# Kernel optimization log

Measured on AMD Instinct MI355X. Metric: run time of the kernel, lower is better.

## Reference

```python
import jax, jax.numpy as jnp
import numpy as np

# LIF dynamics constants (match init_kwargs)
STEPS = 20          # T // dt
DT = 1.0
TAU_M = 20.0
TAU_S = 5.0
THRESH = 1.0
SUR_ALPHA = 10.0    # surrogate-gradient sharpness (stand-in for custom spikeprop bwd)

@jax.custom_vjp
def spike_fn(v):
    # Heaviside threshold; nondifferentiable, custom vjp supplies surrogate grad
    return (v >= THRESH).astype(v.dtype)

def _spike_fwd(v):
    return spike_fn(v), v

def _spike_bwd(v, g):
    # fast-sigmoid (SuperSpike) surrogate derivative centered at threshold
    sur = 1.0 / (1.0 + SUR_ALPHA * jnp.abs(v - THRESH)) ** 2
    return (g * sur,)

spike_fn.defvjp(_spike_fwd, _spike_bwd)


def setup_inputs() -> dict:
    key = jax.random.key(0)
    k1, k2 = jax.random.split(key)
    # Bernoulli(0.1) rate-coded input spike train: [steps, batch, input_dim]
    x = (jax.random.uniform(k1, (STEPS, 512, 2048)) < 0.1).astype(jnp.float32)
    # nn.init.normal_(weight, mean=mu, std=mu) with mu=0.1; W: [output_dim, input_dim]
    W = 0.1 + 0.1 * jax.random.normal(k2, (2048, 2048), dtype=jnp.float32)
    return {"x": x, "W": W}


def reference(x, W):
    # x: [steps, batch, input_dim] spikes; W: [out, in]
    a_m = 1.0 - DT / TAU_M   # membrane decay
    a_s = 1.0 - DT / TAU_S   # synaptic decay
    B = x.shape[1]
    O = W.shape[0]

    def step(carry, x_t):
        V, I = carry                       # [B, O] each
        V_new = a_m * V + (DT / TAU_M) * I # leaky integration of synaptic current
        s = spike_fn(V_new)                # threshold crossing -> spikes
        V_new = V_new * (1.0 - s)          # reset-to-zero on spike
        I_new = a_s * I + x_t @ W.T        # synaptic current driven by input spikes
        return (V_new, I_new), s

    init = (jnp.zeros((B, O), x.dtype), jnp.zeros((B, O), x.dtype))
    _, spikes = jax.lax.scan(step, init, x)
    return spikes  # [steps, batch, output_dim]
```

## Files before the change

kernel.cpp:

```cpp
#include <hip/hip_runtime.h>
#include <stdint.h>


#define STEPS  20
#define BATCH  512
#define DIM    2048

#define XQ_OFF   0ULL
#define WQ_OFF   20971520ULL
#define C_OFF    37748736ULL

#define GLOBAL_AS __attribute__((address_space(1)))
#define LDS_AS    __attribute__((address_space(3)))

typedef int v4i  __attribute__((ext_vector_type(4)));
typedef int v16i __attribute__((ext_vector_type(16)));


__global__ __launch_bounds__(256)
void prep_x_kernel(const float* __restrict__ x, char* __restrict__ wsb)
{
    const int bid = blockIdx.x;
    const int kc = bid & 31, mt = bid >> 5;
    const int tid = threadIdx.x;
    char* outb = wsb + (size_t)bid * 8192;
#pragma unroll
    for (int it = 0; it < 8; ++it) {
        const int idx = it * 256 + tid;
        const int mm = idx >> 4;
        const int kk4 = (idx & 15) << 2;
        const float4 v = *reinterpret_cast<const float4*>(
            x + (size_t)(mt * 128 + mm) * DIM + kc * 64 + kk4);
        uchar4 o;
        o.x = (v.x != 0.0f); o.y = (v.y != 0.0f);
        o.z = (v.z != 0.0f); o.w = (v.w != 0.0f);
        *reinterpret_cast<uchar4*>(
            outb + (((kk4 >> 4) * 128 + mm) << 4) + (kk4 & 15)) = o;
    }
}

__global__ __launch_bounds__(256)
void prep_w_kernel(const float* __restrict__ W, char* __restrict__ wsb)
{
    const int bid = blockIdx.x;
    const int kc = bid & 31, nt = bid >> 5;
    const int tid = threadIdx.x;
    char* wqb = wsb + WQ_OFF;
#pragma unroll
    for (int it = 0; it < 8; ++it) {
        const int idx = it * 256 + tid;
        const int nn = idx >> 4;
        const int kk4 = (idx & 15) << 2;
        const float4 v = *reinterpret_cast<const float4*>(
            W + (size_t)(nt * 128 + nn) * DIM + kc * 64 + kk4);
        int dg[4][4];
        const float* vp = &v.x;
#pragma unroll
        for (int c = 0; c < 4; ++c) {
            long long q = __double2ll_rn((double)vp[c] * 2147483648.0);
#pragma unroll
            for (int j = 0; j < 3; ++j) {
                int d = (int)(q & 255);
                if (d >= 128) d -= 256;
                dg[c][j] = d;
                q = (q - d) >> 8;
            }
            dg[c][3] = (int)q;
        }
        const size_t sub = (size_t)(((kk4 >> 4) * 128 + nn) << 4) + (kk4 & 15);
#pragma unroll
        for (int j = 0; j < 4; ++j) {
            uchar4 o;
            o.x = (unsigned char)(dg[0][j] & 255);
            o.y = (unsigned char)(dg[1][j] & 255);
            o.z = (unsigned char)(dg[2][j] & 255);
            o.w = (unsigned char)(dg[3][j] & 255);
            *reinterpret_cast<uchar4*>(
                wqb + ((size_t)((j * 16 + nt) * 32 + kc)) * 8192 + sub) = o;
        }
    }
}

__global__ __launch_bounds__(256, 4)
void gemm_i8_kernel(const char* __restrict__ wsb_c, short* __restrict__ cp,
                    int nt0, int ntc_cnt, int no)
{
    __shared__ __align__(16) char lds[2][16384];

    const int bid = blockIdx.x;
    const int mt = bid % 80;
    const int rest = bid / 80;
    const int ntc = rest % ntc_cnt;
    const int limb = rest / ntc_cnt;

    const int tid = threadIdx.x;
    const int lane = tid & 63, w = tid >> 6;
    const int kh = lane >> 5, ln = lane & 31;
    const int wy = w & 1, wx = w >> 1;

    const char* abase = wsb_c + XQ_OFF + ((size_t)mt * 32) * 8192;
    const char* bbase = wsb_c + WQ_OFF
        + ((size_t)((limb * 16 + nt0 + ntc) * 32)) * 8192;

    const int aoff = ((kh * 128) + wy * 64 + ln) << 4;
    const int boff = ((kh * 128) + wx * 64 + ln) << 4;
    const int stg = (w * 2) * 1024 + (lane << 4);

    v16i acc00, acc01, acc10, acc11;
#pragma unroll
    for (int r = 0; r < 16; ++r) {
        acc00[r] = 0; acc01[r] = 0; acc10[r] = 0; acc11[r] = 0;
    }

    LDS_AS char* l0 = (LDS_AS char*)(&lds[0][0]);
    LDS_AS char* l1 = (LDS_AS char*)(&lds[1][0]);

#pragma unroll
    for (int i = 0; i < 2; ++i) {
        __builtin_amdgcn_global_load_lds(
            (const GLOBAL_AS void*)(abase + stg + i * 1024),
            (LDS_AS void*)(l0 + (w * 2 + i) * 1024), 16, 0, 0);
        __builtin_amdgcn_global_load_lds(
            (const GLOBAL_AS void*)(bbase + stg + i * 1024),
            (LDS_AS void*)(l0 + 8192 + (w * 2 + i) * 1024), 16, 0, 0);
    }

    for (int kc = 0; kc < 32; ++kc) {
        __syncthreads();
        const int cur = kc & 1;
        if (kc + 1 < 32) {
            LDS_AS char* ldst = (kc & 1) ? l0 : l1;
            const size_t src = (size_t)(kc + 1) * 8192 + stg;
#pragma unroll
            for (int i = 0; i < 2; ++i) {
                __builtin_amdgcn_global_load_lds(
                    (const GLOBAL_AS void*)(abase + src + i * 1024),
                    (LDS_AS void*)(ldst + (w * 2 + i) * 1024), 16, 0, 0);
                __builtin_amdgcn_global_load_lds(
                    (const GLOBAL_AS void*)(bbase + src + i * 1024),
                    (LDS_AS void*)(ldst + 8192 + (w * 2 + i) * 1024), 16, 0, 0);
            }
        }
        const char* A = &lds[cur][0];
        const char* B = &lds[cur][8192];
#pragma unroll
        for (int s = 0; s < 2; ++s) {
            const v4i a0 = *reinterpret_cast<const v4i*>(A + aoff + s * 4096);
            const v4i a1 = *reinterpret_cast<const v4i*>(A + aoff + 512 + s * 4096);
            const v4i b0 = *reinterpret_cast<const v4i*>(B + boff + s * 4096);
            const v4i b1 = *reinterpret_cast<const v4i*>(B + boff + 512 + s * 4096);
            acc00 = __builtin_amdgcn_mfma_i32_32x32x32_i8(a0, b0, acc00, 0, 0, 0);
            acc01 = __builtin_amdgcn_mfma_i32_32x32x32_i8(a0, b1, acc01, 0, 0, 0);
            acc10 = __builtin_amdgcn_mfma_i32_32x32x32_i8(a1, b0, acc10, 0, 0, 0);
            acc11 = __builtin_amdgcn_mfma_i32_32x32x32_i8(a1, b1, acc11, 0, 0, 0);
        }
    }

    short* cpl = cp + (size_t)limb * 10240 * no;
    const int m_base = mt * 128 + wy * 64;
    const int o_base = ntc * 128 + wx * 64 + ln;
#pragma unroll
    for (int r = 0; r < 16; ++r) {
        const int row = (r & 3) + ((r >> 2) << 3) + (kh << 2);
        const size_t m0 = (size_t)(m_base + row) * no;
        const size_t m1 = (size_t)(m_base + 32 + row) * no;
        cpl[m0 + o_base]      = (short)acc00[r];
        cpl[m0 + o_base + 32] = (short)acc01[r];
        cpl[m1 + o_base]      = (short)acc10[r];
        cpl[m1 + o_base + 32] = (short)acc11[r];
    }
}

__global__ __launch_bounds__(256)
void lif_kernel(const short* __restrict__ cp, float* __restrict__ out,
                int o0, int no, int shift)
{
    const int g = blockIdx.x * 256 + threadIdx.x;
    const int b = g >> shift;
    const int oq = g & ((1 << shift) - 1);
    const int o_local = oq << 2;
    const size_t plane = (size_t)10240 * no;

    const double A_M = 1.0 - 1.0 / 20.0;
    const double DTM = 1.0 / 20.0;
    const double A_S = 1.0 - 1.0 / 5.0;
    double V[4], I[4];
#pragma unroll
    for (int u = 0; u < 4; ++u) { V[u] = 0.0; I[u] = 0.0; }

#pragma unroll
    for (int t = 0; t < STEPS; ++t) {
        const size_t ix = (size_t)(t * BATCH + b) * no + o_local;
        const short4 c0 = *reinterpret_cast<const short4*>(cp + ix);
        const short4 c1 = *reinterpret_cast<const short4*>(cp + plane + ix);
        const short4 c2 = *reinterpret_cast<const short4*>(cp + 2 * plane + ix);
        const short4 c3 = *reinterpret_cast<const short4*>(cp + 3 * plane + ix);
        const short* p0 = &c0.x; const short* p1 = &c1.x;
        const short* p2 = &c2.x; const short* p3 = &c3.x;
        float4 s;
        float* sp = &s.x;
#pragma unroll
        for (int u = 0; u < 4; ++u) {
            const long long tot = (long long)p0[u]
                + ((long long)p1[u] << 8)
                + ((long long)p2[u] << 16)
                + ((long long)p3[u] << 24);
            const double val = (double)tot * 4.6566128730773926e-10;
            V[u] = A_M * V[u] + DTM * I[u];
            float sv = 0.0f;
            if (V[u] >= 1.0) { sv = 1.0f; V[u] = 0.0; }
            sp[u] = sv;
            I[u] = A_S * I[u] + val;
        }
        *reinterpret_cast<float4*>(
            out + (size_t)(t * BATCH + b) * DIM + o0 + o_local) = s;
    }
}


#define B_TILE 2
#define O_TILE 256
#define NT     512
#define KT     32
#define NSLAB  (DIM / KT)
#define ROWB   1024

__global__ __launch_bounds__(256)
void transpose_kernel(const float* __restrict__ W, float* __restrict__ WT)
{
    __shared__ float tile[64][65];
    const int tid = threadIdx.x;
    const int c4 = (tid & 15) * 4;
    const int rr = tid >> 4;
    const int k0 = blockIdx.x * 64, o0 = blockIdx.y * 64;
#pragma unroll
    for (int i = 0; i < 64; i += 16) {
        const float4 v = *reinterpret_cast<const float4*>(
            W + (size_t)(o0 + rr + i) * DIM + k0 + c4);
        tile[c4 + 0][rr + i] = v.x;
        tile[c4 + 1][rr + i] = v.y;
        tile[c4 + 2][rr + i] = v.z;
        tile[c4 + 3][rr + i] = v.w;
    }
    __syncthreads();
#pragma unroll
    for (int i = 0; i < 64; i += 16) {
        float4 v;
        v.x = tile[rr + i][c4 + 0];
        v.y = tile[rr + i][c4 + 1];
        v.z = tile[rr + i][c4 + 2];
        v.w = tile[rr + i][c4 + 3];
        *reinterpret_cast<float4*>(
            WT + (size_t)(k0 + rr + i) * DIM + o0 + c4) = v;
    }
}

__global__ __launch_bounds__(NT, 6)
void snn_lif_kernel(const float* __restrict__ x,
                    const float* __restrict__ WT,
                    float* __restrict__ out)
{
    __shared__ __align__(16) float wlds[(KT * ROWB) / 4];

    const int tid  = threadIdx.x;
    const int lane = tid & 63;
    const int w    = tid >> 6;
    const int bl   = w & 1;
    const int tq   = w >> 1;
    const int o_blk = blockIdx.x & 7;
    const int b_blk = blockIdx.x >> 3;
    const int b  = b_blk * B_TILE + bl;
    const int o0 = o_blk * O_TILE;

    double acc[5][4];
#pragma unroll
    for (int tt = 0; tt < 5; ++tt)
#pragma unroll
        for (int u = 0; u < 4; ++u) acc[tt][u] = 0.0;

    const int kl = lane & 31;
    float xr[5];
#pragma unroll
    for (int m = 0; m < 5; ++m)
        xr[m] = x[((size_t)(tq * 5 + m) * BATCH + b) * DIM + kl];

    const char*   gb   = (const char*)wlds + (lane << 4);
    LDS_AS char*  ldsb = (LDS_AS char*)wlds;
    const float*  wsrc = WT + o0 + (lane << 2);

    for (int kt = 0; kt < NSLAB; ++kt) {
        const int k0 = kt * KT;
        __syncthreads();
#pragma unroll
        for (int it = 0; it < 4; ++it) {
            const int r = w + it * 8;
            __builtin_amdgcn_global_load_lds(
                (const GLOBAL_AS void*)(wsrc + (size_t)(k0 + r) * DIM),
                (LDS_AS void*)(ldsb + r * ROWB), 16, 0, 0);
        }
        unsigned mk[5];
#pragma unroll
        for (int m = 0; m < 5; ++m)
            mk[m] = (unsigned)__ballot(xr[m] != 0.0f);
        __syncthreads();
        if (kt + 1 < NSLAB) {
            const int k1 = k0 + KT;
#pragma unroll
            for (int m = 0; m < 5; ++m)
                xr[m] = x[((size_t)(tq * 5 + m) * BATCH + b) * DIM + k1 + kl];
        }
#pragma unroll
        for (int m = 0; m < 5; ++m) {
            unsigned msk = mk[m];
            while (msk & (msk - 1)) {
                const int r0 = __builtin_ctz(msk); msk &= msk - 1;
                const int r1 = __builtin_ctz(msk); msk &= msk - 1;
                const float4 va = *reinterpret_cast<const float4*>(gb + (r0 << 10));
                const float4 vb = *reinterpret_cast<const float4*>(gb + (r1 << 10));
                acc[m][0] += (double)va.x; acc[m][1] += (double)va.y;
                acc[m][2] += (double)va.z; acc[m][3] += (double)va.w;
                acc[m][0] += (double)vb.x; acc[m][1] += (double)vb.y;
                acc[m][2] += (double)vb.z; acc[m][3] += (double)vb.w;
            }
            if (msk) {
                const int r = __builtin_ctz(msk);
                const float4 wv = *reinterpret_cast<const float4*>(gb + (r << 10));
                acc[m][0] += (double)wv.x; acc[m][1] += (double)wv.y;
                acc[m][2] += (double)wv.z; acc[m][3] += (double)wv.w;
            }
        }
    }

    const double A_M = 1.0 - 1.0 / 20.0;
    const double DTM = 1.0 / 20.0;
    const double A_S = 1.0 - 1.0 / 5.0;

    __syncthreads();
    double2* hand = reinterpret_cast<double2*>(wlds);
    const int hbase = bl * 256 + (lane << 2);
    const size_t obase = (size_t)o0 + (lane << 2);

    for (int seg = 0; seg < 4; ++seg) {
        if (tq == seg) {
            double V[4], I[4];
            if (seg == 0) {
#pragma unroll
                for (int u = 0; u < 4; ++u) { V[u] = 0.0; I[u] = 0.0; }
            } else {
#pragma unroll
                for (int u = 0; u < 4; ++u) {
                    const double2 h = hand[hbase + u];
                    V[u] = h.x; I[u] = h.y;
                }
            }
#pragma unroll
            for (int tt = 0; tt < 5; ++tt) {
                const int t = seg * 5 + tt;
                float4 s;
                float* sp = &s.x;
#pragma unroll
                for (int u = 0; u < 4; ++u) {
                    V[u] = A_M * V[u] + DTM * I[u];
                    float sv = 0.0f;
                    if (V[u] >= 1.0) { sv = 1.0f; V[u] = 0.0; }
                    sp[u] = sv;
                    I[u] = A_S * I[u] + acc[tt][u];
                }
                *reinterpret_cast<float4*>(
                    out + ((size_t)t * BATCH + b) * DIM + obase) = s;
            }
            if (seg < 3) {
#pragma unroll
                for (int u = 0; u < 4; ++u)
                    hand[hbase + u] = make_double2(V[u], I[u]);
            }
        }
        __syncthreads();
    }
}


extern "C" void kernel_launch(void* const* d_in, const int* in_sizes, int n_in,
                              void* d_out, int out_size, void* d_ws, size_t ws_size,
                              hipStream_t stream) {
    const float* x = (const float*)d_in[0];
    const float* W = (const float*)d_in[1];
    float* out = (float*)d_out;
    char* wsb = (char*)d_ws;

    int no = 0, shift = 0;
    if      (ws_size >= C_OFF + 81920ULL * 2048) { no = 2048; shift = 9; }
    else if (ws_size >= C_OFF + 81920ULL * 1024) { no = 1024; shift = 8; }
    else if (ws_size >= C_OFF + 81920ULL * 512)  { no = 512;  shift = 7; }
    else if (ws_size >= C_OFF + 81920ULL * 256)  { no = 256;  shift = 6; }
    else if (ws_size >= C_OFF + 81920ULL * 128)  { no = 128;  shift = 5; }

    if (no) {
        prep_x_kernel<<<2560, 256, 0, stream>>>(x, wsb);
        prep_w_kernel<<<512, 256, 0, stream>>>(W, wsb);
        short* cp = (short*)(wsb + C_OFF);
        const int ntc_cnt = no / 128;
        for (int nt0 = 0; nt0 < 16; nt0 += ntc_cnt) {
            gemm_i8_kernel<<<4 * ntc_cnt * 80, 256, 0, stream>>>(
                (const char*)wsb, cp, nt0, ntc_cnt, no);
            lif_kernel<<<no / 2, 256, 0, stream>>>(
                (const short*)cp, out, nt0 * 128, no, shift);
        }
    } else {
        float* WT = (float*)d_ws;
        dim3 tb(256);
        dim3 tg(DIM / 64, DIM / 64);
        transpose_kernel<<<tg, tb, 0, stream>>>(W, WT);
        const int grid = (BATCH / B_TILE) * (DIM / O_TILE);
        snn_lif_kernel<<<grid, NT, 0, stream>>>(x, WT, out);
    }
}
```

Baseline: 338.0 us.

## Enlarge int8 GEMM block tile to 256x128 and stage W-limb writes through LDS

```diff
diff --git a/kernel.cpp b/kernel.cpp
--- a/kernel.cpp
+++ b/kernel.cpp
@@ -42,6 +42,7 @@
 __global__ __launch_bounds__(256)
 void prep_w_kernel(const float* __restrict__ W, char* __restrict__ wsb)
 {
+    __shared__ __align__(16) char pl[4][8192];
     const int bid = blockIdx.x;
     const int kc = bid & 31, nt = bid >> 5;
     const int tid = threadIdx.x;
@@ -67,7 +68,7 @@
             }
             dg[c][3] = (int)q;
         }
-        const size_t sub = (size_t)(((kk4 >> 4) * 128 + nn) << 4) + (kk4 & 15);
+        const int sub = (((kk4 >> 4) * 128 + nn) << 4) + (kk4 & 15);
 #pragma unroll
         for (int j = 0; j < 4; ++j) {
             uchar4 o;
@@ -75,36 +76,48 @@
             o.y = (unsigned char)(dg[1][j] & 255);
             o.z = (unsigned char)(dg[2][j] & 255);
             o.w = (unsigned char)(dg[3][j] & 255);
-            *reinterpret_cast<uchar4*>(
-                wqb + ((size_t)((j * 16 + nt) * 32 + kc)) * 8192 + sub) = o;
-        }
-    }
-}
-
-__global__ __launch_bounds__(256, 4)
+            *reinterpret_cast<uchar4*>(&pl[j][sub]) = o;
+        }
+    }
+    __syncthreads();
+#pragma unroll
+    for (int j = 0; j < 4; ++j) {
+        char* dst = wqb + ((size_t)((j * 16 + nt) * 32 + kc)) * 8192;
+#pragma unroll
+        for (int rep = 0; rep < 2; ++rep) {
+            const int off = (rep * 256 + tid) * 16;
+            *reinterpret_cast<int4*>(dst + off) =
+                *reinterpret_cast<const int4*>(&pl[j][off]);
+        }
+    }
+}
+
+__global__ __launch_bounds__(512, 4)
 void gemm_i8_kernel(const char* __restrict__ wsb_c, short* __restrict__ cp,
                     int nt0, int ntc_cnt, int no)
 {
-    __shared__ __align__(16) char lds[2][16384];
+    __shared__ __align__(16) char lds[2][24576];
 
     const int bid = blockIdx.x;
-    const int mt = bid % 80;
-    const int rest = bid / 80;
+    const int mtb = bid % 40;
+    const int rest = bid / 40;
     const int ntc = rest % ntc_cnt;
     const int limb = rest / ntc_cnt;
 
     const int tid = threadIdx.x;
     const int lane = tid & 63, w = tid >> 6;
     const int kh = lane >> 5, ln = lane & 31;
-    const int wy = w & 1, wx = w >> 1;
-
-    const char* abase = wsb_c + XQ_OFF + ((size_t)mt * 32) * 8192;
+    const int wy = w & 3, wx = w >> 2;
+
+    const char* abase0 = wsb_c + XQ_OFF + ((size_t)(2 * mtb) * 32) * 8192;
+    const char* abase1 = abase0 + (size_t)32 * 8192;
     const char* bbase = wsb_c + WQ_OFF
         + ((size_t)((limb * 16 + nt0 + ntc) * 32)) * 8192;
 
-    const int aoff = ((kh * 128) + wy * 64 + ln) << 4;
-    const int boff = ((kh * 128) + wx * 64 + ln) << 4;
-    const int stg = (w * 2) * 1024 + (lane << 4);
+    const int atile = (wy >> 1) * 8192;
+    const int aoffl = ((kh * 128) + (wy & 1) * 64 + ln) << 4;
+    const int boff  = ((kh * 128) + wx * 64 + ln) << 4;
+    const int stg = w * 1024 + (lane << 4);
 
     v16i acc00, acc01, acc10, acc11;
 #pragma unroll
@@ -115,15 +128,15 @@
     LDS_AS char* l0 = (LDS_AS char*)(&lds[0][0]);
     LDS_AS char* l1 = (LDS_AS char*)(&lds[1][0]);
 
-#pragma unroll
-    for (int i = 0; i < 2; ++i) {
-        __builtin_amdgcn_global_load_lds(
-            (const GLOBAL_AS void*)(abase + stg + i * 1024),
-            (LDS_AS void*)(l0 + (w * 2 + i) * 1024), 16, 0, 0);
-        __builtin_amdgcn_global_load_lds(
-            (const GLOBAL_AS void*)(bbase + stg + i * 1024),
-            (LDS_AS void*)(l0 + 8192 + (w * 2 + i) * 1024), 16, 0, 0);
-    }
+    __builtin_amdgcn_global_load_lds(
+        (const GLOBAL_AS void*)(abase0 + stg),
+        (LDS_AS void*)(l0 + w * 1024), 16, 0, 0);
+    __builtin_amdgcn_global_load_lds(
+        (const GLOBAL_AS void*)(abase1 + stg),
+        (LDS_AS void*)(l0 + 8192 + w * 1024), 16, 0, 0);
+    __builtin_amdgcn_global_load_lds(
+        (const GLOBAL_AS void*)(bbase + stg),
+        (LDS_AS void*)(l0 + 16384 + w * 1024), 16, 0, 0);
 
     for (int kc = 0; kc < 32; ++kc) {
         __syncthreads();
@@ -131,22 +144,22 @@
         if (kc + 1 < 32) {
             LDS_AS char* ldst = (kc & 1) ? l0 : l1;
             const size_t src = (size_t)(kc + 1) * 8192 + stg;
-#pragma unroll
-            for (int i = 0; i < 2; ++i) {
-                __builtin_amdgcn_global_load_lds(
-                    (const GLOBAL_AS void*)(abase + src + i * 1024),
-                    (LDS_AS void*)(ldst + (w * 2 + i) * 1024), 16, 0, 0);
-                __builtin_amdgcn_global_load_lds(
-                    (const GLOBAL_AS void*)(bbase + src + i * 1024),
-                    (LDS_AS void*)(ldst + 8192 + (w * 2 + i) * 1024), 16, 0, 0);
-            }
-        }
-        const char* A = &lds[cur][0];
-        const char* B = &lds[cur][8192];
+            __builtin_amdgcn_global_load_lds(
+                (const GLOBAL_AS void*)(abase0 + src),
+                (LDS_AS void*)(ldst + w * 1024), 16, 0, 0);
+            __builtin_amdgcn_global_load_lds(
+                (const GLOBAL_AS void*)(abase1 + src),
+                (LDS_AS void*)(ldst + 8192 + w * 1024), 16, 0, 0);
+            __builtin_amdgcn_global_load_lds(
+                (const GLOBAL_AS void*)(bbase + src),
+                (LDS_AS void*)(ldst + 16384 + w * 1024), 16, 0, 0);
+        }
+        const char* A = &lds[cur][atile];
+        const char* B = &lds[cur][16384];
 #pragma unroll
         for (int s = 0; s < 2; ++s) {
-            const v4i a0 = *reinterpret_cast<const v4i*>(A + aoff + s * 4096);
-            const v4i a1 = *reinterpret_cast<const v4i*>(A + aoff + 512 + s * 4096);
+            const v4i a0 = *reinterpret_cast<const v4i*>(A + aoffl + s * 4096);
+            const v4i a1 = *reinterpret_cast<const v4i*>(A + aoffl + 512 + s * 4096);
             const v4i b0 = *reinterpret_cast<const v4i*>(B + boff + s * 4096);
             const v4i b1 = *reinterpret_cast<const v4i*>(B + boff + 512 + s * 4096);
             acc00 = __builtin_amdgcn_mfma_i32_32x32x32_i8(a0, b0, acc00, 0, 0, 0);
@@ -157,7 +170,7 @@
     }
 
     short* cpl = cp + (size_t)limb * 10240 * no;
-    const int m_base = mt * 128 + wy * 64;
+    const int m_base = mtb * 256 + wy * 64;
     const int o_base = ntc * 128 + wx * 64 + ln;
 #pragma unroll
     for (int r = 0; r < 16; ++r) {
@@ -401,7 +414,7 @@
         short* cp = (short*)(wsb + C_OFF);
         const int ntc_cnt = no / 128;
         for (int nt0 = 0; nt0 < 16; nt0 += ntc_cnt) {
-            gemm_i8_kernel<<<4 * ntc_cnt * 80, 256, 0, stream>>>(
+            gemm_i8_kernel<<<40 * ntc_cnt * 4, 512, 0, stream>>>(
                 (const char*)wsb, cp, nt0, ntc_cnt, no);
             lif_kernel<<<no / 2, 256, 0, stream>>>(
                 (const short*)cp, out, nt0 * 128, no, shift);
```

New measurement: 328.0 us. -3.0%, faster.
